# Kernel optimization log

Measured on AMD Instinct MI355X. Metric: run time of the kernel, lower is better.

Reference implementation:

```python
import jax, jax.numpy as jnp
import numpy as np

F = 64        # atom feature dim (from Linear(64, 32))
N_RBF = 25    # Gaussian RBF expansion size (standard SchNet 0..5 A)
CUTOFF = 5.0
GAMMA = 10.0  # RBF width parameter: exp(-gamma * (d - mu)^2)


def ssp(x):
    # shifted softplus: ln(0.5 * e^x + 0.5) = softplus(x) - ln 2
    return jax.nn.softplus(x) - jnp.log(2.0).astype(x.dtype)


def setup_inputs() -> dict:
    key = jax.random.key(0)
    ks = jax.random.split(key, 16)
    B, N = 4, 512
    embedding = jax.random.normal(ks[0], (B, N, F), jnp.float32)
    d = jax.random.uniform(ks[1], (B, N, N), jnp.float32) * CUTOFF
    distances = 0.5 * (d + jnp.swapaxes(d, 1, 2))  # symmetric pairwise distances
    s = 0.1
    # 3 stacked interaction blocks
    in2f = jax.random.normal(ks[2], (3, F, F), jnp.float32) * s      # atomwise in->filter (no bias)
    fw1 = jax.random.normal(ks[3], (3, N_RBF, F), jnp.float32) * s   # filter net layer 1
    fb1 = jnp.zeros((3, F), jnp.float32)
    fw2 = jax.random.normal(ks[4], (3, F, F), jnp.float32) * s       # filter net layer 2
    fb2 = jnp.zeros((3, F), jnp.float32)
    f2o = jax.random.normal(ks[5], (3, F, F), jnp.float32) * s       # filter->out atomwise
    f2b = jnp.zeros((3, F), jnp.float32)
    dw = jax.random.normal(ks[6], (3, F, F), jnp.float32) * s        # output atomwise
    db = jnp.zeros((3, F), jnp.float32)
    # readout MLP: Linear(64,32) + SSP + Linear(32,1)
    aw1 = jax.random.normal(ks[7], (F, 32), jnp.float32) * s
    ab1 = jnp.zeros((32,), jnp.float32)
    aw2 = jax.random.normal(ks[8], (32, 1), jnp.float32) * s
    ab2 = jnp.zeros((1,), jnp.float32)
    return dict(embedding=embedding, distances=distances, in2f=in2f, fw1=fw1,
                fb1=fb1, fw2=fw2, fb2=fb2, f2o=f2o, f2b=f2b, dw=dw, db=db,
                aw1=aw1, ab1=ab1, aw2=aw2, ab2=ab2)


def reference(embedding, distances, in2f, fw1, fb1, fw2, fb2, f2o, f2b, dw, db,
              aw1, ab1, aw2, ab2):
    dtype = embedding.dtype
    centers = jnp.linspace(0.0, CUTOFF, N_RBF).astype(dtype)
    # Gaussian RBF expansion of pairwise distances: [B, N, N, N_RBF]
    rbf = jnp.exp(-GAMMA * jnp.square(distances[..., None] - centers))
    x = embedding  # [B, N, F]
    for i in range(3):
        f = x @ in2f[i]  # [B, N, F]
        # filter-generating network on expanded distances -> [B, N, N, F]
        W = ssp(jnp.einsum('bijr,rf->bijf', rbf, fw1[i]) + fb1[i])
        W = W @ fw2[i] + fb2[i]
        # continuous-filter convolution: y_i = sum_j f_j * W_ij
        y = jnp.einsum('bjf,bijf->bif', f, W)
        y = ssp(y @ f2o[i] + f2b[i])
        y = y @ dw[i] + db[i]
        x = x + y  # residual
    h = ssp(x @ aw1 + ab1)   # [B, N, 32]
    return h @ aw2 + ab2     # [B, N, 1]
```

## Files before the change

### kernel.cpp

```cpp
#include <hip/hip_runtime.h>

#define KBIN 128
#define TSTRIDE 68
#define TPSZ  8704
#define FBASE 8704
#define FB2   12800

typedef _Float16 half2v __attribute__((ext_vector_type(2)));

__device__ __forceinline__ float ssp(float x) {
    return fmaxf(x, 0.0f) + log1pf(expf(-fabsf(x))) - 0.69314718055994531f;
}

__device__ __forceinline__ float bclane(float v, int l) {
    return __builtin_bit_cast(float, __builtin_amdgcn_readlane(__builtin_bit_cast(int, v), l));
}

__device__ __forceinline__ unsigned int kaenc(float d) {
    float tv = fminf(fmaxf(d, 0.0f)*25.6f, 127.999f);
    int k = (int)tv;
    float fr = tv - (float)k;
    unsigned short fh = __builtin_bit_cast(unsigned short, (_Float16)fr);
    return ((unsigned int)(k*272) << 16) | (unsigned int)fh;
}

__device__ __forceinline__ float matvec64(const float* __restrict__ ldsA, int base, float xv, int lane) {
    float a0 = 0.f, a1 = 0.f, a2 = 0.f, a3 = 0.f;
    #pragma unroll
    for (int gg = 0; gg < 16; ++gg) {
        const float4 w = *(const float4*)&ldsA[base + lane*64 + (((gg + lane) & 15) << 2)];
        a0 += bclane(xv, gg*4+0) * w.x;
        a1 += bclane(xv, gg*4+1) * w.y;
        a2 += bclane(xv, gg*4+2) * w.z;
        a3 += bclane(xv, gg*4+3) * w.w;
    }
    return (a0 + a1) + (a2 + a3);
}

__device__ __forceinline__ void matvec64x2(const float* __restrict__ ldsA, int base,
                                           float xv0, float xv1, int lane,
                                           float& o0, float& o1) {
    float a0 = 0.f, a1 = 0.f, b0 = 0.f, b1 = 0.f;
    #pragma unroll
    for (int gg = 0; gg < 16; ++gg) {
        const float4 w = *(const float4*)&ldsA[base + lane*64 + (((gg + lane) & 15) << 2)];
        a0 += bclane(xv0, gg*4+0) * w.x;
        a1 += bclane(xv0, gg*4+1) * w.y;
        a0 += bclane(xv0, gg*4+2) * w.z;
        a1 += bclane(xv0, gg*4+3) * w.w;
        b0 += bclane(xv1, gg*4+0) * w.x;
        b1 += bclane(xv1, gg*4+1) * w.y;
        b0 += bclane(xv1, gg*4+2) * w.z;
        b1 += bclane(xv1, gg*4+3) * w.w;
    }
    o0 = a0 + a1;
    o1 = b0 + b1;
}

__device__ __forceinline__ void stageWT4(float* __restrict__ lds, int base, const float* __restrict__ W, int tid) {
    for (int s = tid; s < 1024; s += 512) {
        int quad = s >> 6, g = s & 63;
        float4 v;
        v.x = W[(quad*4+0)*64 + g];
        v.y = W[(quad*4+1)*64 + g];
        v.z = W[(quad*4+2)*64 + g];
        v.w = W[(quad*4+3)*64 + g];
        *(float4*)&lds[base + g*64 + (((quad + g) & 15) << 2)] = v;
    }
}

__global__ __launch_bounds__(512) void schnet_pre0(
    const float* __restrict__ emb,
    const float* __restrict__ in2f,
    const float* __restrict__ fw1, const float* __restrict__ fb1,
    const float* __restrict__ fw2, const float* __restrict__ fb2,
    unsigned short* __restrict__ f_out, unsigned int* __restrict__ Tp_g)
{
    __shared__ float lds[12544];
    const int wg = blockIdx.x, tid = threadIdx.x;
    const int wave = tid >> 6, lane = tid & 63;
    if (wg < 128) {
        stageWT4(lds, 0, in2f, tid);
        __syncthreads();
        int row0 = wg*16 + wave*2;
        size_t ro0 = (size_t)row0*64 + lane;
        size_t ro1 = ro0 + 64;
        float f0, f1;
        matvec64x2(lds, 0, emb[ro0], emb[ro1], lane, f0, f1);
        f_out[ro0] = __builtin_bit_cast(unsigned short, (_Float16)f0);
        f_out[ro1] = __builtin_bit_cast(unsigned short, (_Float16)f1);
    } else {
        int widx = wg - 128;
        int tt = widx / 16;
        int k = (widx % 16)*8 + wave;
        const float* fw1t = fw1 + tt*25*64;
        const float* fw2t = fw2 + tt*64*64;
        for (int s = tid; s < 1600; s += 512) lds[s] = fw1t[s];
        for (int s = tid; s < 4096; s += 512) lds[1600 + s] = fw2t[s];
        if (tid < 64) { lds[5696 + tid] = fb1[tt*64 + tid]; lds[5760 + tid] = fb2[tt*64 + tid]; }
        __syncthreads();
        float T2[2];
        #pragma unroll
        for (int e = 0; e < 2; ++e) {
            float dk = (float)(k + e) * (5.0f/128.0f);
            float h1 = lds[5696 + lane];
            for (int r = 0; r < 25; ++r) {
                float sr = dk - (float)r * (5.0f/24.0f);
                h1 += expf(-10.0f*sr*sr) * lds[r*64 + lane];
            }
            float u = ssp(h1);
            float T = lds[5760 + lane];
            #pragma unroll
            for (int gg = 0; gg < 64; ++gg)
                T += bclane(u, gg) * lds[1600 + gg*64 + lane];
            T2[e] = T;
        }
        float* sc = &lds[5824 + wave*128];
        sc[lane] = T2[0];
        sc[64 + lane] = T2[1];
        if (lane < 16) {
            float4 A  = *(const float4*)&sc[lane*4];
            float4 Bv = *(const float4*)&sc[64 + lane*4];
            half2v t01 = { (_Float16)A.x, (_Float16)A.y };
            half2v t23 = { (_Float16)A.z, (_Float16)A.w };
            half2v d01 = { (_Float16)(Bv.x - A.x), (_Float16)(Bv.y - A.y) };
            half2v d23 = { (_Float16)(Bv.z - A.z), (_Float16)(Bv.w - A.w) };
            uint4 o;
            o.x = __builtin_bit_cast(unsigned int, t01);
            o.y = __builtin_bit_cast(unsigned int, t23);
            o.z = __builtin_bit_cast(unsigned int, d01);
            o.w = __builtin_bit_cast(unsigned int, d23);
            *(uint4*)&Tp_g[(size_t)tt*TPSZ + k*TSTRIDE + lane*4] = o;
        }
    }
}

__global__ __launch_bounds__(512, 4) void schnet_block(
    int t,
    const float* __restrict__ emb, const float* __restrict__ dists,
    const float* __restrict__ in2f,
    const float* __restrict__ f2o, const float* __restrict__ f2b,
    const float* __restrict__ dw,  const float* __restrict__ db,
    const float* __restrict__ aw1, const float* __restrict__ ab1,
    const float* __restrict__ aw2, const float* __restrict__ ab2,
    const unsigned int* __restrict__ Tp_g,
    unsigned int* __restrict__ ka,
    const unsigned short* __restrict__ f_in,
    unsigned short* __restrict__ f_out,
    float* __restrict__ x_buf, float* __restrict__ out)
{
    __shared__ unsigned int ldsu[FB2 + 4096];
    float* lds = (float*)ldsu;
    const int wg = blockIdx.x, tid = threadIdx.x;
    const int wave = tid >> 6, lane = tid & 63;
    const int b = wg >> 7, it = wg & 127;
    const int i0 = it * 4;
    const int fq = lane & 15, g = lane >> 4;
    const int r = wave >> 1;
    const int jhalf = wave & 1;

    const unsigned int* Tp = Tp_g + (size_t)t*TPSZ;
    for (int s = tid; s < TPSZ/4; s += 512)
        ((uint4*)ldsu)[s] = ((const uint4*)Tp)[s];

    if (t == 0) {
        int erow = tid >> 7;
        int ecol = (tid & 127) * 4;
        size_t ep = ((size_t)(b*512 + i0 + erow))*512 + ecol;
        float4 dv = *(const float4*)&dists[ep];
        uint4 eo;
        eo.x = kaenc(dv.x); eo.y = kaenc(dv.y); eo.z = kaenc(dv.z); eo.w = kaenc(dv.w);
        *(uint4*)&ka[ep] = eo;
    }

    const int j0 = tid >> 4, fq2 = tid & 15;
    const uint2* fsrc0 = (const uint2*)f_in + ((size_t)b*512 + j0)*16 + fq2;
    const int fo_base = (j0 >> 1)*64 + fq2*4 + (j0 & 1)*2;
    unsigned int* fdstA = ldsu + FBASE + fo_base;
    unsigned int* fdstB = ldsu + FB2 + fo_base;
    const unsigned int* kabase = &ka[((size_t)(b*512 + i0 + r))*512 + jhalf*64 + g*16];

    uint2 rb0, rb1, rb2, rb3;
    uint4 kc0, kc1, kc2, kc3, kn0, kn1, kn2, kn3;
    {
        rb0 = fsrc0[0]; rb1 = fsrc0[512]; rb2 = fsrc0[1024]; rb3 = fsrc0[1536];
        if (t > 0) {
            kc0 = ((const uint4*)kabase)[0];
            kc1 = ((const uint4*)kabase)[1];
            kc2 = ((const uint4*)kabase)[2];
            kc3 = ((const uint4*)kabase)[3];
        }
        *(uint2*)fdstA = rb0; *(uint2*)(fdstA + 1024) = rb1;
        *(uint2*)(fdstA + 2048) = rb2; *(uint2*)(fdstA + 3072) = rb3;
    }
    __syncthreads();
    if (t == 0) {
        kc0 = ((const uint4*)kabase)[0];
        kc1 = ((const uint4*)kabase)[1];
        kc2 = ((const uint4*)kabase)[2];
        kc3 = ((const uint4*)kabase)[3];
    }

    const unsigned int* fpA = ldsu + FBASE + fq*4;
    const unsigned int* fpB = ldsu + FB2 + fq*4;
    const char* Tbyte = (const char*)ldsu + fq*16;
    const int jpb = jhalf*32 + g*8;
    float a0 = 0.f, a1 = 0.f, a2 = 0.f, a3 = 0.f;

    #pragma unroll
    for (int c = 0; c < 4; ++c) {
        if (c < 3) {
            const uint2* sp = fsrc0 + (size_t)(c + 1)*2048;
            rb0 = sp[0]; rb1 = sp[512]; rb2 = sp[1024]; rb3 = sp[1536];
            const uint4* kp = (const uint4*)(kabase + (c + 1)*128);
            kn0 = kp[0]; kn1 = kp[1]; kn2 = kp[2]; kn3 = kp[3];
        }
        const unsigned int* fp = (c & 1) ? fpB : fpA;
        uint4 kqa[4] = {kc0, kc1, kc2, kc3};
        #pragma unroll
        for (int j4 = 0; j4 < 4; ++j4) {
            uint4 fA = *(const uint4*)&fp[(jpb + j4*2)*64];
            uint4 fB = *(const uint4*)&fp[(jpb + j4*2 + 1)*64];
            unsigned int kk[4] = {kqa[j4].x, kqa[j4].y, kqa[j4].z, kqa[j4].w};
            unsigned int fl_[8] = {fA.x, fA.y, fA.z, fA.w, fB.x, fB.y, fB.z, fB.w};
            #pragma unroll
            for (int u = 0; u < 4; ++u) {
                unsigned int kau = kk[u];
                unsigned int koff = kau >> 16;
                half2v av = __builtin_bit_cast(half2v, __builtin_amdgcn_perm(kau, kau, 0x01000100u));
                uint4 tp = *(const uint4*)(Tbyte + koff);
                half2v W01 = __builtin_bit_cast(half2v, tp.z)*av + __builtin_bit_cast(half2v, tp.x);
                half2v W23 = __builtin_bit_cast(half2v, tp.w)*av + __builtin_bit_cast(half2v, tp.y);
                half2v f01 = __builtin_bit_cast(half2v, fl_[u*2]);
                half2v f23 = __builtin_bit_cast(half2v, fl_[u*2+1]);
                a0 += (float)W01[0] * (float)f01[0];
                a1 += (float)W01[1] * (float)f01[1];
                a2 += (float)W23[0] * (float)f23[0];
                a3 += (float)W23[1] * (float)f23[1];
            }
        }
        if (c < 3) {
            unsigned int* fd = (c & 1) ? fdstA : fdstB;
            *(uint2*)fd = rb0; *(uint2*)(fd + 1024) = rb1;
            *(uint2*)(fd + 2048) = rb2; *(uint2*)(fd + 3072) = rb3;
            kc0 = kn0; kc1 = kn1; kc2 = kn2; kc3 = kn3;
            __syncthreads();
        }
    }
    a0 += __shfl_xor(a0, 16, 64); a0 += __shfl_xor(a0, 32, 64);
    a1 += __shfl_xor(a1, 16, 64); a1 += __shfl_xor(a1, 32, 64);
    a2 += __shfl_xor(a2, 16, 64); a2 += __shfl_xor(a2, 32, 64);
    a3 += __shfl_xor(a3, 16, 64); a3 += __shfl_xor(a3, 32, 64);

    __syncthreads();
    if (g == 0) {
        float4 acc; acc.x = a0; acc.y = a1; acc.z = a2; acc.w = a3;
        *(float4*)&lds[FB2 + wave*64 + fq*4] = acc;
    }
    stageWT4(lds, 0, f2o + t*4096, tid);
    stageWT4(lds, 4096, dw + t*4096, tid);
    if (t < 2) {
        stageWT4(lds, 8192, in2f + (t+1)*4096, tid);
    } else {
        for (int s = tid; s < 1024; s += 512) {
            int quad = s >> 6, rr = s & 63;
            float4 v;
            v.x = aw1[(quad*4+0)*32 + (rr & 31)];
            v.y = aw1[(quad*4+1)*32 + (rr & 31)];
            v.z = aw1[(quad*4+2)*32 + (rr & 31)];
            v.w = aw1[(quad*4+3)*32 + (rr & 31)];
            *(float4*)&lds[8192 + rr*64 + (((quad + rr) & 15) << 2)] = v;
        }
    }
    if (tid < 64) {
        lds[12288 + tid] = f2b[t*64 + tid];
        lds[12352 + tid] = db[t*64 + tid];
        if (t == 2) {
            lds[12416 + tid] = ab1[tid & 31];
            lds[12480 + tid] = aw2[tid & 31];
        }
    }
    __syncthreads();

    if (wave < 4) {
        int grow = b*512 + i0 + wave;
        size_t ro = (size_t)grow*64 + lane;
        float y = lds[FB2 + (wave*2)*64 + lane] + lds[FB2 + (wave*2+1)*64 + lane];
        float z = matvec64(lds, 0, y, lane) + lds[12288 + lane];
        float u = ssp(z);
        float y3 = matvec64(lds, 4096, u, lane) + lds[12352 + lane];
        float xin = (t == 0) ? emb[ro] : x_buf[ro];
        float xn = xin + y3;
        if (t < 2) {
            x_buf[ro] = xn;
            float fo = matvec64(lds, 8192, xn, lane);
            f_out[ro] = __builtin_bit_cast(unsigned short, (_Float16)fo);
        } else {
            float s1 = matvec64(lds, 8192, xn, lane) + lds[12416 + lane];
            float h = ssp(s1) * lds[12480 + lane];
            #pragma unroll
            for (int m = 1; m < 64; m <<= 1)
                h += __shfl_xor(h, m, 64);
            if (lane == 0) out[grow] = ab2[0] + 0.5f*h;
        }
    }
}

extern "C" void kernel_launch(void* const* d_in, const int* in_sizes, int n_in,
                              void* d_out, int out_size, void* d_ws, size_t ws_size,
                              hipStream_t stream) {
    const float* emb  = (const float*)d_in[0];
    const float* dist = (const float*)d_in[1];
    const float* in2f = (const float*)d_in[2];
    const float* fw1  = (const float*)d_in[3];
    const float* fb1  = (const float*)d_in[4];
    const float* fw2  = (const float*)d_in[5];
    const float* fb2  = (const float*)d_in[6];
    const float* f2o  = (const float*)d_in[7];
    const float* f2b  = (const float*)d_in[8];
    const float* dwp  = (const float*)d_in[9];
    const float* dbp  = (const float*)d_in[10];
    const float* aw1  = (const float*)d_in[11];
    const float* ab1  = (const float*)d_in[12];
    const float* aw2  = (const float*)d_in[13];
    const float* ab2  = (const float*)d_in[14];
    float* out = (float*)d_out;
    float* ws = (float*)d_ws;
    unsigned int* Tp_g = (unsigned int*)ws;
    unsigned short* fA = (unsigned short*)(ws + 26112);
    unsigned short* fB = (unsigned short*)(ws + 26112 + 65536);
    float* x_buf = ws + 26112 + 2*65536;
    unsigned int* ka = (unsigned int*)(x_buf + 131072);

    hipLaunchKernelGGL(schnet_pre0, dim3(176), dim3(512), 0, stream,
        emb, in2f, fw1, fb1, fw2, fb2, fA, Tp_g);
    hipLaunchKernelGGL(schnet_block, dim3(512), dim3(512), 0, stream,
        0, emb, dist, in2f, f2o, f2b, dwp, dbp, aw1, ab1, aw2, ab2,
        Tp_g, ka, fA, fB, x_buf, out);
    hipLaunchKernelGGL(schnet_block, dim3(512), dim3(512), 0, stream,
        1, emb, dist, in2f, f2o, f2b, dwp, dbp, aw1, ab1, aw2, ab2,
        Tp_g, ka, fB, fA, x_buf, out);
    hipLaunchKernelGGL(schnet_block, dim3(512), dim3(512), 0, stream,
        2, emb, dist, in2f, f2o, f2b, dwp, dbp, aw1, ab1, aw2, ab2,
        Tp_g, ka, fA, fB, x_buf, out);
}
```

Measured before the change: 61.81 us.

## Split row work so each wave handles two rows over a quarter of j

Reassigns the wave decomposition: instead of each wave owning one row i and half the j range, each wave now processes two rows over a quarter of j. Each f vector loaded from LDS is reused for two rows, halving f reads per FMA. The cost is twice as many accumulators per thread, a four-way cross-wave reduction in the epilogue, and a larger scratch area in shared memory.

```diff
diff --git a/kernel.cpp b/kernel.cpp
--- a/kernel.cpp
+++ b/kernel.cpp
@@ -5,6 +5,7 @@
 #define TPSZ  8704
 #define FBASE 8704
 #define FB2   12800
+#define YSCR  12800
 
 typedef _Float16 half2v __attribute__((ext_vector_type(2)));
 
@@ -156,8 +157,8 @@
     const int b = wg >> 7, it = wg & 127;
     const int i0 = it * 4;
     const int fq = lane & 15, g = lane >> 4;
-    const int r = wave >> 1;
-    const int jhalf = wave & 1;
+    const int rp = wave & 1;
+    const int jq = wave >> 1;
 
     const unsigned int* Tp = Tp_g + (size_t)t*TPSZ;
     for (int s = tid; s < TPSZ/4; s += 512)
@@ -178,84 +179,104 @@
     const int fo_base = (j0 >> 1)*64 + fq2*4 + (j0 & 1)*2;
     unsigned int* fdstA = ldsu + FBASE + fo_base;
     unsigned int* fdstB = ldsu + FB2 + fo_base;
-    const unsigned int* kabase = &ka[((size_t)(b*512 + i0 + r))*512 + jhalf*64 + g*16];
+    const unsigned int* kab0 = &ka[((size_t)(b*512 + i0 + 2*rp))*512 + jq*32 + g*8];
+    const unsigned int* kab1 = kab0 + 512;
 
     uint2 rb0, rb1, rb2, rb3;
-    uint4 kc0, kc1, kc2, kc3, kn0, kn1, kn2, kn3;
+    uint4 kc00, kc01, kc10, kc11, kn00, kn01, kn10, kn11;
     {
         rb0 = fsrc0[0]; rb1 = fsrc0[512]; rb2 = fsrc0[1024]; rb3 = fsrc0[1536];
         if (t > 0) {
-            kc0 = ((const uint4*)kabase)[0];
-            kc1 = ((const uint4*)kabase)[1];
-            kc2 = ((const uint4*)kabase)[2];
-            kc3 = ((const uint4*)kabase)[3];
+            kc00 = ((const uint4*)kab0)[0]; kc01 = ((const uint4*)kab0)[1];
+            kc10 = ((const uint4*)kab1)[0]; kc11 = ((const uint4*)kab1)[1];
         }
         *(uint2*)fdstA = rb0; *(uint2*)(fdstA + 1024) = rb1;
         *(uint2*)(fdstA + 2048) = rb2; *(uint2*)(fdstA + 3072) = rb3;
     }
     __syncthreads();
     if (t == 0) {
-        kc0 = ((const uint4*)kabase)[0];
-        kc1 = ((const uint4*)kabase)[1];
-        kc2 = ((const uint4*)kabase)[2];
-        kc3 = ((const uint4*)kabase)[3];
+        kc00 = ((const uint4*)kab0)[0]; kc01 = ((const uint4*)kab0)[1];
+        kc10 = ((const uint4*)kab1)[0]; kc11 = ((const uint4*)kab1)[1];
     }
 
     const unsigned int* fpA = ldsu + FBASE + fq*4;
     const unsigned int* fpB = ldsu + FB2 + fq*4;
     const char* Tbyte = (const char*)ldsu + fq*16;
-    const int jpb = jhalf*32 + g*8;
-    float a0 = 0.f, a1 = 0.f, a2 = 0.f, a3 = 0.f;
+    const int jpb = jq*16 + g*4;
+    float a00 = 0.f, a01 = 0.f, a02 = 0.f, a03 = 0.f;
+    float a10 = 0.f, a11 = 0.f, a12 = 0.f, a13 = 0.f;
 
     #pragma unroll
     for (int c = 0; c < 4; ++c) {
         if (c < 3) {
             const uint2* sp = fsrc0 + (size_t)(c + 1)*2048;
             rb0 = sp[0]; rb1 = sp[512]; rb2 = sp[1024]; rb3 = sp[1536];
-            const uint4* kp = (const uint4*)(kabase + (c + 1)*128);
-            kn0 = kp[0]; kn1 = kp[1]; kn2 = kp[2]; kn3 = kp[3];
+            const uint4* kp0 = (const uint4*)(kab0 + (c + 1)*128);
+            const uint4* kp1 = (const uint4*)(kab1 + (c + 1)*128);
+            kn00 = kp0[0]; kn01 = kp0[1];
+            kn10 = kp1[0]; kn11 = kp1[1];
         }
         const unsigned int* fp = (c & 1) ? fpB : fpA;
-        uint4 kqa[4] = {kc0, kc1, kc2, kc3};
+        uint4 k0a[2] = {kc00, kc01};
+        uint4 k1a[2] = {kc10, kc11};
         #pragma unroll
-        for (int j4 = 0; j4 < 4; ++j4) {
+        for (int j4 = 0; j4 < 2; ++j4) {
             uint4 fA = *(const uint4*)&fp[(jpb + j4*2)*64];
             uint4 fB = *(const uint4*)&fp[(jpb + j4*2 + 1)*64];
-            unsigned int kk[4] = {kqa[j4].x, kqa[j4].y, kqa[j4].z, kqa[j4].w};
+            unsigned int kk0[4] = {k0a[j4].x, k0a[j4].y, k0a[j4].z, k0a[j4].w};
+            unsigned int kk1[4] = {k1a[j4].x, k1a[j4].y, k1a[j4].z, k1a[j4].w};
             unsigned int fl_[8] = {fA.x, fA.y, fA.z, fA.w, fB.x, fB.y, fB.z, fB.w};
             #pragma unroll
             for (int u = 0; u < 4; ++u) {
-                unsigned int kau = kk[u];
-                unsigned int koff = kau >> 16;
-                half2v av = __builtin_bit_cast(half2v, __builtin_amdgcn_perm(kau, kau, 0x01000100u));
-                uint4 tp = *(const uint4*)(Tbyte + koff);
-                half2v W01 = __builtin_bit_cast(half2v, tp.z)*av + __builtin_bit_cast(half2v, tp.x);
-                half2v W23 = __builtin_bit_cast(half2v, tp.w)*av + __builtin_bit_cast(half2v, tp.y);
                 half2v f01 = __builtin_bit_cast(half2v, fl_[u*2]);
                 half2v f23 = __builtin_bit_cast(half2v, fl_[u*2+1]);
-                a0 += (float)W01[0] * (float)f01[0];
-                a1 += (float)W01[1] * (float)f01[1];
-                a2 += (float)W23[0] * (float)f23[0];
-                a3 += (float)W23[1] * (float)f23[1];
+                {
+                    unsigned int kau = kk0[u];
+                    half2v av = __builtin_bit_cast(half2v, __builtin_amdgcn_perm(kau, kau, 0x01000100u));
+                    uint4 tp = *(const uint4*)(Tbyte + (kau >> 16));
+                    half2v W01 = __builtin_bit_cast(half2v, tp.z)*av + __builtin_bit_cast(half2v, tp.x);
+                    half2v W23 = __builtin_bit_cast(half2v, tp.w)*av + __builtin_bit_cast(half2v, tp.y);
+                    a00 += (float)W01[0] * (float)f01[0];
+                    a01 += (float)W01[1] * (float)f01[1];
+                    a02 += (float)W23[0] * (float)f23[0];
+                    a03 += (float)W23[1] * (float)f23[1];
+                }
+                {
+                    unsigned int kau = kk1[u];
+                    half2v av = __builtin_bit_cast(half2v, __builtin_amdgcn_perm(kau, kau, 0x01000100u));
+                    uint4 tp = *(const uint4*)(Tbyte + (kau >> 16));
+                    half2v W01 = __builtin_bit_cast(half2v, tp.z)*av + __builtin_bit_cast(half2v, tp.x);
+                    half2v W23 = __builtin_bit_cast(half2v, tp.w)*av + __builtin_bit_cast(half2v, tp.y);
+                    a10 += (float)W01[0] * (float)f01[0];
+                    a11 += (float)W01[1] * (float)f01[1];
+                    a12 += (float)W23[0] * (float)f23[0];
+                    a13 += (float)W23[1] * (float)f23[1];
+                }
             }
         }
         if (c < 3) {
             unsigned int* fd = (c & 1) ? fdstA : fdstB;
             *(uint2*)fd = rb0; *(uint2*)(fd + 1024) = rb1;
             *(uint2*)(fd + 2048) = rb2; *(uint2*)(fd + 3072) = rb3;
-            kc0 = kn0; kc1 = kn1; kc2 = kn2; kc3 = kn3;
+            kc00 = kn00; kc01 = kn01; kc10 = kn10; kc11 = kn11;
             __syncthreads();
         }
     }
-    a0 += __shfl_xor(a0, 16, 64); a0 += __shfl_xor(a0, 32, 64);
-    a1 += __shfl_xor(a1, 16, 64); a1 += __shfl_xor(a1, 32, 64);
-    a2 += __shfl_xor(a2, 16, 64); a2 += __shfl_xor(a2, 32, 64);
-    a3 += __shfl_xor(a3, 16, 64); a3 += __shfl_xor(a3, 32, 64);
+    a00 += __shfl_xor(a00, 16, 64); a00 += __shfl_xor(a00, 32, 64);
+    a01 += __shfl_xor(a01, 16, 64); a01 += __shfl_xor(a01, 32, 64);
+    a02 += __shfl_xor(a02, 16, 64); a02 += __shfl_xor(a02, 32, 64);
+    a03 += __shfl_xor(a03, 16, 64); a03 += __shfl_xor(a03, 32, 64);
+    a10 += __shfl_xor(a10, 16, 64); a10 += __shfl_xor(a10, 32, 64);
+    a11 += __shfl_xor(a11, 16, 64); a11 += __shfl_xor(a11, 32, 64);
+    a12 += __shfl_xor(a12, 16, 64); a12 += __shfl_xor(a12, 32, 64);
+    a13 += __shfl_xor(a13, 16, 64); a13 += __shfl_xor(a13, 32, 64);
 
     __syncthreads();
     if (g == 0) {
-        float4 acc; acc.x = a0; acc.y = a1; acc.z = a2; acc.w = a3;
-        *(float4*)&lds[FB2 + wave*64 + fq*4] = acc;
+        float4 r0; r0.x = a00; r0.y = a01; r0.z = a02; r0.w = a03;
+        float4 r1; r1.x = a10; r1.y = a11; r1.z = a12; r1.w = a13;
+        *(float4*)&lds[YSCR + wave*128 + fq*4] = r0;
+        *(float4*)&lds[YSCR + wave*128 + 64 + fq*4] = r1;
     }
     stageWT4(lds, 0, f2o + t*4096, tid);
     stageWT4(lds, 4096, dw + t*4096, tid);
@@ -283,9 +304,14 @@
     __syncthreads();
 
     if (wave < 4) {
-        int grow = b*512 + i0 + wave;
+        int rt = wave;
+        int grow = b*512 + i0 + rt;
         size_t ro = (size_t)grow*64 + lane;
-        float y = lds[FB2 + (wave*2)*64 + lane] + lds[FB2 + (wave*2+1)*64 + lane];
+        int wbase = (rt >> 1);
+        float y = lds[YSCR + (wbase + 0)*128 + (rt & 1)*64 + lane]
+                + lds[YSCR + (wbase + 2)*128 + (rt & 1)*64 + lane]
+                + lds[YSCR + (wbase + 4)*128 + (rt & 1)*64 + lane]
+                + lds[YSCR + (wbase + 6)*128 + (rt & 1)*64 + lane];
         float z = matvec64(lds, 0, y, lane) + lds[12288 + lane];
         float u = ssp(z);
         float y3 = matvec64(lds, 4096, u, lane) + lds[12352 + lane];
```

After: 60.12 us, median of 2. 1.03x faster.

## Have each wave cover all four rows over a j-slice to reuse f loads

Applied to the files above, without the earlier changes.

The work split changes from two waves per atom row, each handling half the neighbours, to every wave handling all four rows over its own slice of neighbours. Each loaded f vector is then reused across four rows, which cuts LDS traffic for f. The ka loads are no longer prefetched one chunk ahead but are issued inside each chunk, and each lane now holds 16 accumulators. The partial sums from the eight waves are reduced through LDS scratch, which adds register pressure and a larger final reduction.

```diff
diff --git a/kernel.cpp b/kernel.cpp
--- a/kernel.cpp
+++ b/kernel.cpp
@@ -5,6 +5,7 @@
 #define TPSZ  8704
 #define FBASE 8704
 #define FB2   12800
+#define YSCR  12800
 
 typedef _Float16 half2v __attribute__((ext_vector_type(2)));
 
@@ -156,8 +157,6 @@
     const int b = wg >> 7, it = wg & 127;
     const int i0 = it * 4;
     const int fq = lane & 15, g = lane >> 4;
-    const int r = wave >> 1;
-    const int jhalf = wave & 1;
 
     const unsigned int* Tp = Tp_g + (size_t)t*TPSZ;
     for (int s = tid; s < TPSZ/4; s += 512)
@@ -178,84 +177,86 @@
     const int fo_base = (j0 >> 1)*64 + fq2*4 + (j0 & 1)*2;
     unsigned int* fdstA = ldsu + FBASE + fo_base;
     unsigned int* fdstB = ldsu + FB2 + fo_base;
-    const unsigned int* kabase = &ka[((size_t)(b*512 + i0 + r))*512 + jhalf*64 + g*16];
+    const unsigned int* kab = &ka[((size_t)(b*512 + i0))*512 + wave*16 + g*4];
 
     uint2 rb0, rb1, rb2, rb3;
-    uint4 kc0, kc1, kc2, kc3, kn0, kn1, kn2, kn3;
     {
         rb0 = fsrc0[0]; rb1 = fsrc0[512]; rb2 = fsrc0[1024]; rb3 = fsrc0[1536];
-        if (t > 0) {
-            kc0 = ((const uint4*)kabase)[0];
-            kc1 = ((const uint4*)kabase)[1];
-            kc2 = ((const uint4*)kabase)[2];
-            kc3 = ((const uint4*)kabase)[3];
-        }
         *(uint2*)fdstA = rb0; *(uint2*)(fdstA + 1024) = rb1;
         *(uint2*)(fdstA + 2048) = rb2; *(uint2*)(fdstA + 3072) = rb3;
     }
     __syncthreads();
-    if (t == 0) {
-        kc0 = ((const uint4*)kabase)[0];
-        kc1 = ((const uint4*)kabase)[1];
-        kc2 = ((const uint4*)kabase)[2];
-        kc3 = ((const uint4*)kabase)[3];
-    }
 
     const unsigned int* fpA = ldsu + FBASE + fq*4;
     const unsigned int* fpB = ldsu + FB2 + fq*4;
     const char* Tbyte = (const char*)ldsu + fq*16;
-    const int jpb = jhalf*32 + g*8;
-    float a0 = 0.f, a1 = 0.f, a2 = 0.f, a3 = 0.f;
+    const int jpb = wave*8 + g*2;
+    float acc[4][4];
+    #pragma unroll
+    for (int r = 0; r < 4; ++r)
+        #pragma unroll
+        for (int q = 0; q < 4; ++q) acc[r][q] = 0.f;
 
     #pragma unroll
     for (int c = 0; c < 4; ++c) {
         if (c < 3) {
             const uint2* sp = fsrc0 + (size_t)(c + 1)*2048;
             rb0 = sp[0]; rb1 = sp[512]; rb2 = sp[1024]; rb3 = sp[1536];
-            const uint4* kp = (const uint4*)(kabase + (c + 1)*128);
-            kn0 = kp[0]; kn1 = kp[1]; kn2 = kp[2]; kn3 = kp[3];
-        }
+        }
+        const unsigned int* kap = kab + c*128;
+        uint4 kr0 = *(const uint4*)(kap);
+        uint4 kr1 = *(const uint4*)(kap + 512);
+        uint4 kr2 = *(const uint4*)(kap + 1024);
+        uint4 kr3 = *(const uint4*)(kap + 1536);
+        unsigned int kk[4][4] = {
+            {kr0.x, kr0.y, kr0.z, kr0.w},
+            {kr1.x, kr1.y, kr1.z, kr1.w},
+            {kr2.x, kr2.y, kr2.z, kr2.w},
+            {kr3.x, kr3.y, kr3.z, kr3.w}};
         const unsigned int* fp = (c & 1) ? fpB : fpA;
-        uint4 kqa[4] = {kc0, kc1, kc2, kc3};
-        #pragma unroll
-        for (int j4 = 0; j4 < 4; ++j4) {
-            uint4 fA = *(const uint4*)&fp[(jpb + j4*2)*64];
-            uint4 fB = *(const uint4*)&fp[(jpb + j4*2 + 1)*64];
-            unsigned int kk[4] = {kqa[j4].x, kqa[j4].y, kqa[j4].z, kqa[j4].w};
-            unsigned int fl_[8] = {fA.x, fA.y, fA.z, fA.w, fB.x, fB.y, fB.z, fB.w};
+        uint4 fA = *(const uint4*)&fp[jpb*64];
+        uint4 fB = *(const uint4*)&fp[(jpb + 1)*64];
+        unsigned int fl_[8] = {fA.x, fA.y, fA.z, fA.w, fB.x, fB.y, fB.z, fB.w};
+        #pragma unroll
+        for (int u = 0; u < 4; ++u) {
+            half2v f01 = __builtin_bit_cast(half2v, fl_[u*2]);
+            half2v f23 = __builtin_bit_cast(half2v, fl_[u*2+1]);
             #pragma unroll
-            for (int u = 0; u < 4; ++u) {
-                unsigned int kau = kk[u];
-                unsigned int koff = kau >> 16;
+            for (int r = 0; r < 4; ++r) {
+                unsigned int kau = kk[r][u];
                 half2v av = __builtin_bit_cast(half2v, __builtin_amdgcn_perm(kau, kau, 0x01000100u));
-                uint4 tp = *(const uint4*)(Tbyte + koff);
+                uint4 tp = *(const uint4*)(Tbyte + (kau >> 16));
                 half2v W01 = __builtin_bit_cast(half2v, tp.z)*av + __builtin_bit_cast(half2v, tp.x);
                 half2v W23 = __builtin_bit_cast(half2v, tp.w)*av + __builtin_bit_cast(half2v, tp.y);
-                half2v f01 = __builtin_bit_cast(half2v, fl_[u*2]);
-                half2v f23 = __builtin_bit_cast(half2v, fl_[u*2+1]);
-                a0 += (float)W01[0] * (float)f01[0];
-                a1 += (float)W01[1] * (float)f01[1];
-                a2 += (float)W23[0] * (float)f23[0];
-                a3 += (float)W23[1] * (float)f23[1];
+                acc[r][0] += (float)W01[0] * (float)f01[0];
+                acc[r][1] += (float)W01[1] * (float)f01[1];
+                acc[r][2] += (float)W23[0] * (float)f23[0];
+                acc[r][3] += (float)W23[1] * (float)f23[1];
             }
         }
         if (c < 3) {
             unsigned int* fd = (c & 1) ? fdstA : fdstB;
             *(uint2*)fd = rb0; *(uint2*)(fd + 1024) = rb1;
             *(uint2*)(fd + 2048) = rb2; *(uint2*)(fd + 3072) = rb3;
-            kc0 = kn0; kc1 = kn1; kc2 = kn2; kc3 = kn3;
             __syncthreads();
         }
     }
-    a0 += __shfl_xor(a0, 16, 64); a0 += __shfl_xor(a0, 32, 64);
-    a1 += __shfl_xor(a1, 16, 64); a1 += __shfl_xor(a1, 32, 64);
-    a2 += __shfl_xor(a2, 16, 64); a2 += __shfl_xor(a2, 32, 64);
-    a3 += __shfl_xor(a3, 16, 64); a3 += __shfl_xor(a3, 32, 64);
+    #pragma unroll
+    for (int r = 0; r < 4; ++r) {
+        #pragma unroll
+        for (int q = 0; q < 4; ++q) {
+            acc[r][q] += __shfl_xor(acc[r][q], 16, 64);
+            acc[r][q] += __shfl_xor(acc[r][q], 32, 64);
+        }
+    }
 
     __syncthreads();
     if (g == 0) {
-        float4 acc; acc.x = a0; acc.y = a1; acc.z = a2; acc.w = a3;
-        *(float4*)&lds[FB2 + wave*64 + fq*4] = acc;
+        #pragma unroll
+        for (int r = 0; r < 4; ++r) {
+            float4 rv; rv.x = acc[r][0]; rv.y = acc[r][1]; rv.z = acc[r][2]; rv.w = acc[r][3];
+            *(float4*)&lds[YSCR + wave*256 + r*64 + fq*4] = rv;
+        }
     }
     stageWT4(lds, 0, f2o + t*4096, tid);
     stageWT4(lds, 4096, dw + t*4096, tid);
@@ -283,9 +284,13 @@
     __syncthreads();
 
     if (wave < 4) {
-        int grow = b*512 + i0 + wave;
+        int rt = wave;
+        int grow = b*512 + i0 + rt;
         size_t ro = (size_t)grow*64 + lane;
-        float y = lds[FB2 + (wave*2)*64 + lane] + lds[FB2 + (wave*2+1)*64 + lane];
+        float y = 0.f;
+        #pragma unroll
+        for (int w = 0; w < 8; ++w)
+            y += lds[YSCR + w*256 + rt*64 + lane];
         float z = matvec64(lds, 0, y, lane) + lds[12288 + lane];
         float u = ssp(z);
         float y3 = matvec64(lds, 4096, u, lane) + lds[12352 + lane];
```

Result: slower. 73.06 us (+18.2%).
